# Kernel optimization log

Measured on AMD Instinct MI355X. Metric: run time of the kernel, lower is better.

## Reference

```python
import jax, jax.numpy as jnp
import numpy as np
from jax.ops import segment_sum

N = 100000      # nodes
E = 1600000     # edges
G = 128         # graphs in batch
D = 128         # input (embedding) dim
H = 128         # hidden dim
WALK = 16       # random-walk length
PED = 16        # PE embed dim
L = 5           # GNN layers
OUT = 10        # classes
EPS = 1e-5      # batchnorm eps


def setup_inputs() -> dict:
    key = jax.random.key(0)
    ks = jax.random.split(key, 32)
    f = lambda k, shp: (jax.random.normal(k, shp, dtype=jnp.float32) * 0.05)
    inp = {
        'x': jnp.zeros((N,), dtype=jnp.int64) if jax.config.jax_enable_x64 else jnp.zeros((N,), dtype=jnp.int32),
        'edge_index': jax.random.randint(ks[0], (2, E), 0, N),
        'batch': jnp.sort(jax.random.randint(ks[1], (N,), 0, G)),
        'emb_table': f(ks[2], (1, D)),
        'pe_w': f(ks[3], (WALK, PED)), 'pe_b': f(ks[4], (PED,)),
        'proj_w': f(ks[5], (D + PED, H)), 'proj_b': f(ks[6], (H,)),
        'gin_w1': f(ks[7], (L, H, H)), 'gin_b1': f(ks[8], (L, H)),
        'gin_w2': f(ks[9], (L, H, H)), 'gin_b2': f(ks[10], (L, H)),
        'bn_g': jnp.ones((L, H), jnp.float32), 'bn_b': jnp.zeros((L, H), jnp.float32),
        'ffn_w1': f(ks[11], (L, H, 2 * H)), 'ffn_b1': f(ks[12], (L, 2 * H)),
        'ffn_w2': f(ks[13], (L, 2 * H, H)), 'ffn_b2': f(ks[14], (L, H)),
        'ffn_bn_g': jnp.ones((L, H), jnp.float32), 'ffn_bn_b': jnp.zeros((L, H), jnp.float32),
        'out_w1': f(ks[15], (H, H)), 'out_b1': f(ks[16], (H,)),
        'out_w2': f(ks[17], (H, OUT)), 'out_b2': f(ks[18], (OUT,)),
    }
    return inp


def _batchnorm(h, g, b):
    # BatchNorm1d forward with batch statistics (training-mode math)
    mu = jnp.mean(h, axis=0)
    var = jnp.var(h, axis=0)
    return (h - mu) * jax.lax.rsqrt(var + EPS) * g + b


def _forward(emb_table, pe_w, pe_b, proj_w, proj_b, gin_w1, gin_b1, gin_w2, gin_b2,
             bn_g, bn_b, ffn_w1, ffn_b1, ffn_w2, ffn_b2, ffn_bn_g, ffn_bn_b,
             out_w1, out_b1, out_w2, out_b2, x, edge_index, batch):
    h0 = emb_table[x]                                # [N, D] (all indices are 0)

    # ---- RandomWalkPositionalEncoding (vectorized scatter-add per step) ----
    row0, col0 = edge_index[0], edge_index[1]
    loops = jnp.arange(N)
    row = jnp.concatenate([row0, loops])
    col = jnp.concatenate([col0, loops])             # self loops appended
    deg = segment_sum(jnp.ones(row.shape, jnp.float32), col, num_segments=N)
    dinv = jnp.where(deg > 0, jax.lax.rsqrt(jnp.maximum(deg, 1.0)), 0.0)
    norm_e = dinv[row] * dinv[col]                   # [E+N]

    cnt = segment_sum(jnp.ones((N,), jnp.float32), batch, num_segments=G)
    prob = 1.0 / jnp.maximum(cnt, 1.0)[batch]        # per-graph uniform init

    def rw_step(p, _):
        new_p = segment_sum(p[row] * norm_e, col, num_segments=N)
        return new_p * 0.9 + p * 0.1, p

    _, rw = jax.lax.scan(rw_step, prob, None, length=WALK)   # [WALK, N]
    pe = rw.T @ pe_w + pe_b                          # [N, PED]

    # ---- input projection ----
    h = jnp.concatenate([h0, pe], axis=-1) @ proj_w + proj_b # [N, H]

    # ---- stacked GIN layers with BN, residual and FFN (dropout = eval identity) ----
    for i in range(L):
        res = h
        agg = segment_sum(h[row0], col0, num_segments=N) + h  # GIN: (1+eps)x + sum_j x_j, eps=0
        z = jax.nn.relu(agg @ gin_w1[i] + gin_b1[i]) @ gin_w2[i] + gin_b2[i]
        z = jax.nn.relu(_batchnorm(z, bn_g[i], bn_b[i]))
        h = z + res
        res2 = h
        f = jax.nn.relu(h @ ffn_w1[i] + ffn_b1[i]) @ ffn_w2[i] + ffn_b2[i]
        h = _batchnorm(f + res2, ffn_bn_g[i], ffn_bn_b[i])

    # ---- global mean pooling + MLP head ----
    gsum = segment_sum(h, batch, num_segments=G)
    g = gsum / jnp.maximum(cnt, 1.0)[:, None]        # [G, H]
    out = jax.nn.relu(g @ out_w1 + out_b1) @ out_w2 + out_b2
    return out                                        # [G, OUT]


def reference(x, edge_index, batch, emb_table, pe_w, pe_b, proj_w, proj_b,
              gin_w1, gin_b1, gin_w2, gin_b2, bn_g, bn_b, ffn_w1, ffn_b1,
              ffn_w2, ffn_b2, ffn_bn_g, ffn_bn_b, out_w1, out_b1, out_w2, out_b2):
    return _forward(emb_table, pe_w, pe_b, proj_w, proj_b, gin_w1, gin_b1, gin_w2,
                    gin_b2, bn_g, bn_b, ffn_w1, ffn_b1, ffn_w2, ffn_b2,
                    ffn_bn_g, ffn_bn_b, out_w1, out_b1, out_w2, out_b2,
                    x, edge_index, batch)
```

## Files before the change

### kernel.cpp

```cpp
#include <hip/hip_runtime.h>
#include <math.h>

#define NN 100000
#define NE 1600000
#define NG 128
#define HD 128
#define WLK 16
#define NL 5
#define NOUT 10
#define BNEPS 1e-5f
#define CDIV(a,b) (((a)+(b)-1)/(b))

#define NBKT 782
#define NEB 400
#define EPB 4000
#define NSCAN (NBKT*NEB)
#define NSB CDIV(NSCAN,1024)
#define NBM 782

typedef float f32x4 __attribute__((ext_vector_type(4)));
typedef _Float16 f16x8 __attribute__((ext_vector_type(8)));
typedef unsigned short ushort_t;
typedef unsigned int uint_t;

__device__ __forceinline__ ushort_t f2h(float x) {
    union { _Float16 h; ushort_t u; } c;
    c.h = (_Float16)x;
    return c.u;
}
__device__ __forceinline__ float h2f(ushort_t u) {
    union { ushort_t u; _Float16 h; } c;
    c.u = u;
    return (float)c.h;
}

__global__ void k_cnt(const int* __restrict__ batch, int* __restrict__ cnt,
                      int* __restrict__ goff) {
    int g = threadIdx.x;
    if (g >= NG) return;
    int lo0 = 0, hi0 = NN;
    while (lo0 < hi0) { int m = (lo0 + hi0) >> 1; if (batch[m] < g) lo0 = m + 1; else hi0 = m; }
    int lo1 = lo0, hi1 = NN;
    while (lo1 < hi1) { int m = (lo1 + hi1) >> 1; if (batch[m] < g + 1) lo1 = m + 1; else hi1 = m; }
    cnt[g] = lo1 - lo0;
    goff[g] = lo0;
}

__global__ void k_bhist(const int* __restrict__ col0, int* __restrict__ bhist) {
    __shared__ int hist[NBKT];
    for (int i = threadIdx.x; i < NBKT; i += 256) hist[i] = 0;
    __syncthreads();
    int e0 = blockIdx.x * EPB;
    for (int e = e0 + threadIdx.x; e < e0 + EPB; e += 256) atomicAdd(&hist[col0[e] >> 7], 1);
    __syncthreads();
    for (int i = threadIdx.x; i < NBKT; i += 256) bhist[i * NEB + blockIdx.x] = hist[i];
}

__global__ void k_gscan1(const int* __restrict__ in, int* __restrict__ bsum) {
    __shared__ int sm[256];
    int base = blockIdx.x * 1024 + threadIdx.x * 4;
    int s = 0;
#pragma unroll
    for (int i = 0; i < 4; ++i) { int e = base + i; if (e < NSCAN) s += in[e]; }
    sm[threadIdx.x] = s; __syncthreads();
    for (int st = 128; st > 0; st >>= 1) {
        if (threadIdx.x < st) sm[threadIdx.x] += sm[threadIdx.x + st];
        __syncthreads();
    }
    if (threadIdx.x == 0) bsum[blockIdx.x] = sm[0];
}

__global__ void k_scan2(int* __restrict__ blksum, int nblk) {
    __shared__ int sm[512];
    int t = threadIdx.x;
    int x = (t < nblk) ? blksum[t] : 0;
    sm[t] = x; __syncthreads();
    for (int s = 1; s < 512; s <<= 1) {
        int v = (t >= s) ? sm[t - s] : 0;
        __syncthreads();
        sm[t] += v;
        __syncthreads();
    }
    if (t < nblk) blksum[t] = sm[t] - x;
}

__global__ void k_gscan3(const int* __restrict__ in, const int* __restrict__ bsum,
                         int* __restrict__ out) {
    __shared__ int sm[256];
    int t = threadIdx.x;
    int base = blockIdx.x * 1024 + t * 4;
    int v[4]; int s = 0;
#pragma unroll
    for (int i = 0; i < 4; ++i) { int e = base + i; v[i] = (e < NSCAN) ? in[e] : 0; s += v[i]; }
    sm[t] = s; __syncthreads();
    for (int st = 1; st < 256; st <<= 1) {
        int x = (t >= st) ? sm[t - st] : 0;
        __syncthreads();
        sm[t] += x;
        __syncthreads();
    }
    int excl = sm[t] - s + bsum[blockIdx.x];
#pragma unroll
    for (int i = 0; i < 4; ++i) { int e = base + i; if (e < NSCAN) { out[e] = excl; excl += v[i]; } }
}

__global__ void k_escatter(const int* __restrict__ row0, const int* __restrict__ col0,
                           const int* __restrict__ boffs, int2* __restrict__ epair) {
    __shared__ int cur[NBKT];
    for (int i = threadIdx.x; i < NBKT; i += 256) cur[i] = boffs[i * NEB + blockIdx.x];
    __syncthreads();
    int e0 = blockIdx.x * EPB;
    for (int e = e0 + threadIdx.x; e < e0 + EPB; e += 256) {
        int c = col0[e], r = row0[e];
        int pos = atomicAdd(&cur[c >> 7], 1);
        epair[pos] = make_int2(c, r);
    }
}

__global__ void k_bucket(const int2* __restrict__ epair, const int* __restrict__ boffs,
                         int* __restrict__ rowptr, int* __restrict__ deg,
                         int* __restrict__ esrc) {
    __shared__ int cnt_[128], scn[128], cur_[128];
    int bkt = blockIdx.x, t = threadIdx.x;
    int bs = boffs[bkt * NEB];
    int be = (bkt + 1 < NBKT) ? boffs[(bkt + 1) * NEB] : NE;
    if (t < 128) cnt_[t] = 0;
    __syncthreads();
    for (int e = bs + t; e < be; e += 256) atomicAdd(&cnt_[epair[e].x & 127], 1);
    __syncthreads();
    int c = (t < 128) ? cnt_[t] : 0;
    if (t < 128) scn[t] = c;
    __syncthreads();
    for (int st = 1; st < 128; st <<= 1) {
        int x = (t >= st && t < 128) ? scn[t - st] : 0;
        __syncthreads();
        if (t < 128) scn[t] += x;
        __syncthreads();
    }
    if (t < 128) {
        int excl = scn[t] - c;
        int node = bkt * 128 + t;
        if (node < NN) { rowptr[node] = bs + excl; deg[node] = c; }
        cur_[t] = bs + excl;
    }
    if (bkt == NBKT - 1 && t == 0) rowptr[NN] = NE;
    __syncthreads();
    for (int e = bs + t; e < be; e += 256) {
        int2 p = epair[e];
        int pos = atomicAdd(&cur_[p.x & 127], 1);
        esrc[pos] = p.y;
    }
}

__global__ void k_init_pe(const int* __restrict__ deg, const int* __restrict__ batch,
                          const int* __restrict__ cnt, float* __restrict__ dinv,
                          float* __restrict__ p, float* __restrict__ pd) {
    int v = blockIdx.x * 256 + threadIdx.x;
    if (v >= NN) return;
    float dv = rsqrtf((float)(deg[v] + 1));
    dinv[v] = dv;
    float pv = 1.0f / fmaxf((float)cnt[batch[v]], 1.0f);
    p[v] = pv; pd[v] = pv * dv;
}

__global__ void k_rw_step(const float* __restrict__ pin, const float* __restrict__ pdin,
                          const int* __restrict__ rowptr, const int* __restrict__ esrc,
                          const float* __restrict__ dinv, float* __restrict__ rwslice,
                          float* __restrict__ pout, float* __restrict__ pdout) {
    int v = blockIdx.x * 256 + threadIdx.x;
    if (v >= NN) return;
    int b = rowptr[v], e = rowptr[v + 1];
    float a[8];
#pragma unroll
    for (int k = 0; k < 8; ++k) a[k] = 0.f;
    int i = b;
    for (; i + 8 <= e; i += 8) {
        int s[8];
#pragma unroll
        for (int k = 0; k < 8; ++k) s[k] = esrc[i + k];
#pragma unroll
        for (int k = 0; k < 8; ++k) a[k] += pdin[s[k]];
    }
    for (; i < e; ++i) a[0] += pdin[esrc[i]];
    float s = ((a[0] + a[1]) + (a[2] + a[3])) + ((a[4] + a[5]) + (a[6] + a[7]));
    float dv = dinv[v];
    float pv = pin[v];
    float np = s * dv + pv * dv * dv;
    float nxt = 0.9f * np + 0.1f * pv;
    rwslice[v] = pv;
    pout[v] = nxt;
    pdout[v] = nxt * dv;
}

__global__ void k_mc1(const float* __restrict__ emb, const float* __restrict__ pe_w,
                      const float* __restrict__ pe_b, const float* __restrict__ proj_w,
                      const float* __restrict__ proj_b, float* __restrict__ M,
                      float* __restrict__ c1, float* __restrict__ bnA0,
                      float* __restrict__ bnB0) {
    int j = threadIdx.x;
    bnA0[j] = 1.f; bnB0[j] = 0.f;
    float c0 = proj_b[j];
    for (int d = 0; d < HD; ++d) c0 += emb[d] * proj_w[d * HD + j];
    for (int w = 0; w < WLK; ++w) c0 += pe_b[w] * proj_w[(HD + w) * HD + j];
    c1[j] = c0;
    for (int s = 0; s < WLK; ++s) {
        float m = 0.f;
        for (int w = 0; w < WLK; ++w) m += pe_w[s * WLK + w] * proj_w[(HD + w) * HD + j];
        M[s * HD + j] = m;
    }
}

__global__ void k_proj(const float* __restrict__ rw, const float* __restrict__ M,
                       const float* __restrict__ c1, uint2* __restrict__ th4) {
    int idx = blockIdx.x * 256 + threadIdx.x;
    if (idx >= NN * 32) return;
    int v = idx >> 5, cg = (idx & 31) * 4;
    float4 acc = *(const float4*)&c1[cg];
#pragma unroll
    for (int s = 0; s < WLK; ++s) {
        float r = rw[s * NN + v];
        float4 m = *(const float4*)&M[s * HD + cg];
        acc.x += r * m.x; acc.y += r * m.y; acc.z += r * m.z; acc.w += r * m.w;
    }
    th4[idx] = make_uint2((uint_t)f2h(acc.x) | ((uint_t)f2h(acc.y) << 16),
                          (uint_t)f2h(acc.z) | ((uint_t)f2h(acc.w) << 16));
}

__global__ void k_prepw(const float* __restrict__ g1, const float* __restrict__ g2,
                        const float* __restrict__ f1, const float* __restrict__ f2,
                        ushort_t* __restrict__ wt1, ushort_t* __restrict__ wt2,
                        ushort_t* __restrict__ wt3, ushort_t* __restrict__ wt4) {
    int i = blockIdx.x * 256 + threadIdx.x;
    if (i < 81920) {
        int l = i >> 14, rem = i & 16383, n = rem >> 7, k = rem & 127;
        wt1[i] = f2h(g1[l * 16384 + k * 128 + n]);
    } else if (i < 163840) {
        int j = i - 81920;
        int l = j >> 14, rem = j & 16383, n = rem >> 7, k = rem & 127;
        wt2[j] = f2h(g2[l * 16384 + k * 128 + n]);
    } else if (i < 327680) {
        int j = i - 163840;
        int l = j >> 15, rem = j & 32767, n = rem >> 7, k = rem & 127;
        wt3[j] = f2h(f1[l * 32768 + k * 256 + n]);
    } else {
        int j = i - 327680;
        int l = j >> 15, rem = j & 32767, n = rem >> 8, k = rem & 255;
        wt4[j] = f2h(f2[l * 32768 + k * 128 + n]);
    }
}

__global__ void k_aggb(const uint_t* __restrict__ th2, const int* __restrict__ rowptr,
                       const int* __restrict__ esrc, const float* __restrict__ bnA0,
                       const float* __restrict__ bnB0, uint_t* __restrict__ aggb2) {
    int wave = threadIdx.x >> 6, lane = threadIdx.x & 63;
    int v = blockIdx.x * 4 + wave;
    if (v >= NN) return;
    uint_t u = th2[(size_t)v * 64 + lane];
    float sx[8], sy[8];
#pragma unroll
    for (int k = 0; k < 8; ++k) { sx[k] = 0.f; sy[k] = 0.f; }
    sx[0] = h2f((ushort_t)(u & 0xFFFFu)); sy[0] = h2f((ushort_t)(u >> 16));
    int b = rowptr[v], e = rowptr[v + 1];
    int i = b;
    for (; i + 8 <= e; i += 8) {
        int idx[8]; uint_t x[8];
#pragma unroll
        for (int k = 0; k < 8; ++k) idx[k] = esrc[i + k];
#pragma unroll
        for (int k = 0; k < 8; ++k) x[k] = th2[(size_t)idx[k] * 64 + lane];
#pragma unroll
        for (int k = 0; k < 8; ++k) {
            sx[k] += h2f((ushort_t)(x[k] & 0xFFFFu));
            sy[k] += h2f((ushort_t)(x[k] >> 16));
        }
    }
    for (; i < e; ++i) {
        uint_t x = th2[(size_t)esrc[i] * 64 + lane];
        sx[0] += h2f((ushort_t)(x & 0xFFFFu)); sy[0] += h2f((ushort_t)(x >> 16));
    }
    float fx = ((sx[0] + sx[1]) + (sx[2] + sx[3])) + ((sx[4] + sx[5]) + (sx[6] + sx[7]));
    float fy = ((sy[0] + sy[1]) + (sy[2] + sy[3])) + ((sy[4] + sy[5]) + (sy[6] + sy[7]));
    float2 A = *(const float2*)&bnA0[lane * 2];
    float2 B = *(const float2*)&bnB0[lane * 2];
    float cf = (float)(e - b + 1);
    float ox = A.x * fx + cf * B.x;
    float oy = A.y * fy + cf * B.y;
    aggb2[(size_t)v * 64 + lane] = (uint_t)f2h(ox) | ((uint_t)f2h(oy) << 16);
}

#define GLDK 136
__global__ __launch_bounds__(256)
void k_gin(const ushort_t* __restrict__ A, const ushort_t* __restrict__ W1T,
           const ushort_t* __restrict__ W2T, const float* __restrict__ b1,
           const float* __restrict__ b2, ushort_t* __restrict__ z2h,
           float* __restrict__ partS, float* __restrict__ partQ) {
    __shared__ ushort_t As[128 * GLDK];
    __shared__ ushort_t Ws[64 * GLDK];
    __shared__ float sS[128], sQ[128];
    const int tid = threadIdx.x;
    const int w = tid >> 6, l = tid & 63;
    const int lm = l & 15, lq = l >> 4;
    const int rw0 = w * 32;
    const int vr0 = blockIdx.x * 128;
    if (tid < 128) { sS[tid] = 0.f; sQ[tid] = 0.f; }

#pragma unroll
    for (int it = 0; it < 8; ++it) {
        int f = it * 256 + tid;
        int row = f >> 4, sl = f & 15;
        uint4 a = make_uint4(0, 0, 0, 0);
        int vr = vr0 + row;
        if (vr < NN) a = *(const uint4*)&A[(size_t)vr * HD + sl * 8];
        *(uint4*)&As[row * GLDK + sl * 8] = a;
    }

    f32x4 z1a[2][2][4] = {};
    for (int c = 0; c < 2; ++c) {
        __syncthreads();
#pragma unroll
        for (int it = 0; it < 4; ++it) {
            int f = it * 256 + tid;
            int row = f >> 4, sl = f & 15;
            *(uint4*)&Ws[row * GLDK + sl * 8] =
                *(const uint4*)&W1T[(size_t)(c * 64 + row) * HD + sl * 8];
        }
        __syncthreads();
#pragma unroll
        for (int kk = 0; kk < 128; kk += 32) {
            f16x8 af[2], bf[4];
#pragma unroll
            for (int i = 0; i < 2; ++i)
                af[i] = *(const f16x8*)&As[(rw0 + i * 16 + lm) * GLDK + kk + lq * 8];
#pragma unroll
            for (int j = 0; j < 4; ++j)
                bf[j] = *(const f16x8*)&Ws[(j * 16 + lm) * GLDK + kk + lq * 8];
#pragma unroll
            for (int i = 0; i < 2; ++i)
#pragma unroll
                for (int j = 0; j < 4; ++j)
                    z1a[c][i][j] = __builtin_amdgcn_mfma_f32_16x16x32_f16(af[i], bf[j], z1a[c][i][j], 0, 0, 0);
        }
    }
    __syncthreads();

#pragma unroll
    for (int c = 0; c < 2; ++c)
#pragma unroll
        for (int j = 0; j < 4; ++j) {
            int col = c * 64 + j * 16 + lm;
            float bj = b1[col];
#pragma unroll
            for (int i = 0; i < 2; ++i)
#pragma unroll
                for (int r = 0; r < 4; ++r) {
                    int row = rw0 + i * 16 + lq * 4 + r;
                    As[row * GLDK + col] = f2h(fmaxf(z1a[c][i][j][r] + bj, 0.f));
                }
        }

    f32x4 z2a[2][2][4] = {};
    for (int c2 = 0; c2 < 2; ++c2) {
        __syncthreads();
#pragma unroll
        for (int it = 0; it < 4; ++it) {
            int f = it * 256 + tid;
            int row = f >> 4, sl = f & 15;
            *(uint4*)&Ws[row * GLDK + sl * 8] =
                *(const uint4*)&W2T[(size_t)(c2 * 64 + row) * HD + sl * 8];
        }
        __syncthreads();
#pragma unroll
        for (int kk = 0; kk < 128; kk += 32) {
            f16x8 af[2], bf[4];
#pragma unroll
            for (int i = 0; i < 2; ++i)
                af[i] = *(const f16x8*)&As[(rw0 + i * 16 + lm) * GLDK + kk + lq * 8];
#pragma unroll
            for (int j = 0; j < 4; ++j)
                bf[j] = *(const f16x8*)&Ws[(j * 16 + lm) * GLDK + kk + lq * 8];
#pragma unroll
            for (int i = 0; i < 2; ++i)
#pragma unroll
                for (int j = 0; j < 4; ++j)
                    z2a[c2][i][j] = __builtin_amdgcn_mfma_f32_16x16x32_f16(af[i], bf[j], z2a[c2][i][j], 0, 0, 0);
        }
    }

    float ls[2][4] = {}, lsq[2][4] = {};
#pragma unroll
    for (int c2 = 0; c2 < 2; ++c2)
#pragma unroll
        for (int j = 0; j < 4; ++j) {
            int col = c2 * 64 + j * 16 + lm;
            float bj = b2[col];
#pragma unroll
            for (int i = 0; i < 2; ++i)
#pragma unroll
                for (int r = 0; r < 4; ++r) {
                    int vr = vr0 + rw0 + i * 16 + lq * 4 + r;
                    if (vr < NN) {
                        float x = z2a[c2][i][j][r] + bj;
                        ls[c2][j] += x; lsq[c2][j] += x * x;
                        z2h[(size_t)vr * HD + col] = f2h(x);
                    }
                }
        }
#pragma unroll
    for (int c2 = 0; c2 < 2; ++c2)
#pragma unroll
        for (int j = 0; j < 4; ++j) {
            atomicAdd(&sS[c2 * 64 + j * 16 + lm], ls[c2][j]);
            atomicAdd(&sQ[c2 * 64 + j * 16 + lm], lsq[c2][j]);
        }
    __syncthreads();
    if (tid < 128) {
        partS[(size_t)tid * NBM + blockIdx.x] = sS[tid];
        partQ[(size_t)tid * NBM + blockIdx.x] = sQ[tid];
    }
}

#define FLDK 72
__global__ __launch_bounds__(256)
void k_ffn(ushort_t* __restrict__ th, const ushort_t* __restrict__ z2h,
           const ushort_t* __restrict__ W3T, const float* __restrict__ b3,
           const ushort_t* __restrict__ W4T, const float* __restrict__ b4,
           const float* __restrict__ bnA0, const float* __restrict__ bnB0,
           const float* __restrict__ bnA1, const float* __restrict__ bnB1,
           float* __restrict__ partS, float* __restrict__ partQ) {
    __shared__ ushort_t As[128 * GLDK];
    __shared__ ushort_t Fs[128 * FLDK];
    __shared__ ushort_t Ws[128 * FLDK];
    __shared__ float sS[128], sQ[128];
    __shared__ float sA0[128], sB0[128], sA1[128], sB1[128];
    const int tid = threadIdx.x;
    const int w = tid >> 6, l = tid & 63;
    const int lm = l & 15, lq = l >> 4;
    const int rw0 = w * 32;
    const int vr0 = blockIdx.x * 128;

    if (tid < 128) {
        sS[tid] = 0.f; sQ[tid] = 0.f;
        sA0[tid] = bnA0[tid]; sB0[tid] = bnB0[tid];
        sA1[tid] = bnA1[tid]; sB1[tid] = bnB1[tid];
    }
    __syncthreads();

#pragma unroll
    for (int it = 0; it < 8; ++it) {
        int f = it * 256 + tid;
        int row = f >> 4, sl = f & 15;
        int vr = vr0 + row;
        uint4 o = make_uint4(0, 0, 0, 0);
        if (vr < NN) {
            uint4 tv = *(const uint4*)&th[(size_t)vr * HD + sl * 8];
            uint4 zv = *(const uint4*)&z2h[(size_t)vr * HD + sl * 8];
            uint_t tu[4] = {tv.x, tv.y, tv.z, tv.w};
            uint_t zu[4] = {zv.x, zv.y, zv.z, zv.w};
            uint_t ou[4];
#pragma unroll
            for (int m = 0; m < 4; ++m) {
                int ch0 = sl * 8 + m * 2;
                float t0 = h2f((ushort_t)(tu[m] & 0xFFFFu));
                float t1 = h2f((ushort_t)(tu[m] >> 16));
                float z0 = h2f((ushort_t)(zu[m] & 0xFFFFu));
                float z1 = h2f((ushort_t)(zu[m] >> 16));
                float h0 = sA0[ch0] * t0 + sB0[ch0] + fmaxf(sA1[ch0] * z0 + sB1[ch0], 0.f);
                float h1 = sA0[ch0 + 1] * t1 + sB0[ch0 + 1] + fmaxf(sA1[ch0 + 1] * z1 + sB1[ch0 + 1], 0.f);
                ou[m] = (uint_t)f2h(h0) | ((uint_t)f2h(h1) << 16);
            }
            o = make_uint4(ou[0], ou[1], ou[2], ou[3]);
        }
        *(uint4*)&As[row * GLDK + sl * 8] = o;
    }

    f32x4 acc2[2][2][4] = {};
    for (int kc = 0; kc < 4; ++kc) {
        __syncthreads();
#pragma unroll
        for (int it = 0; it < 4; ++it) {
            int f = it * 256 + tid;
            int row = f >> 4, sl = f & 15;
            *(uint4*)&Ws[row * GLDK + sl * 8] =
                *(const uint4*)&W3T[(size_t)(kc * 64 + row) * HD + sl * 8];
        }
        __syncthreads();
        f32x4 f1a[2][4] = {};
#pragma unroll
        for (int kk = 0; kk < 128; kk += 32) {
            f16x8 af[2], bf[4];
#pragma unroll
            for (int i = 0; i < 2; ++i)
                af[i] = *(const f16x8*)&As[(rw0 + i * 16 + lm) * GLDK + kk + lq * 8];
#pragma unroll
            for (int j = 0; j < 4; ++j)
                bf[j] = *(const f16x8*)&Ws[(j * 16 + lm) * GLDK + kk + lq * 8];
#pragma unroll
            for (int i = 0; i < 2; ++i)
#pragma unroll
                for (int j = 0; j < 4; ++j)
                    f1a[i][j] = __builtin_amdgcn_mfma_f32_16x16x32_f16(af[i], bf[j], f1a[i][j], 0, 0, 0);
        }
#pragma unroll
        for (int j = 0; j < 4; ++j) {
            int fcol = j * 16 + lm;
            float bj = b3[kc * 64 + fcol];
#pragma unroll
            for (int i = 0; i < 2; ++i)
#pragma unroll
                for (int r = 0; r < 4; ++r) {
                    int row = rw0 + i * 16 + lq * 4 + r;
                    Fs[row * FLDK + fcol] = f2h(fmaxf(f1a[i][j][r] + bj, 0.f));
                }
        }
        __syncthreads();
#pragma unroll
        for (int it = 0; it < 4; ++it) {
            int f = it * 256 + tid;
            int row = f >> 3, sl = f & 7;
            *(uint4*)&Ws[row * FLDK + sl * 8] =
                *(const uint4*)&W4T[(size_t)row * 256 + kc * 64 + sl * 8];
        }
        __syncthreads();
#pragma unroll
        for (int kk = 0; kk < 64; kk += 32) {
            f16x8 af[2];
#pragma unroll
            for (int i = 0; i < 2; ++i)
                af[i] = *(const f16x8*)&Fs[(rw0 + i * 16 + lm) * FLDK + kk + lq * 8];
#pragma unroll
            for (int c2 = 0; c2 < 2; ++c2)
#pragma unroll
                for (int j = 0; j < 4; ++j) {
                    f16x8 bf = *(const f16x8*)&Ws[(c2 * 64 + j * 16 + lm) * FLDK + kk + lq * 8];
#pragma unroll
                    for (int i = 0; i < 2; ++i)
                        acc2[c2][i][j] = __builtin_amdgcn_mfma_f32_16x16x32_f16(af[i], bf, acc2[c2][i][j], 0, 0, 0);
                }
        }
    }

    float ls[2][4] = {}, lsq[2][4] = {};
#pragma unroll
    for (int c2 = 0; c2 < 2; ++c2)
#pragma unroll
        for (int j = 0; j < 4; ++j) {
            int col = c2 * 64 + j * 16 + lm;
            float bj = b4[col];
#pragma unroll
            for (int i = 0; i < 2; ++i)
#pragma unroll
                for (int r = 0; r < 4; ++r) {
                    int lrow = rw0 + i * 16 + lq * 4 + r;
                    int vr = vr0 + lrow;
                    if (vr < NN) {
                        float resv = h2f(As[lrow * GLDK + col]);
                        float x = acc2[c2][i][j][r] + bj + resv;
                        ls[c2][j] += x; lsq[c2][j] += x * x;
                        th[(size_t)vr * HD + col] = f2h(x);
                    }
                }
        }
#pragma unroll
    for (int c2 = 0; c2 < 2; ++c2)
#pragma unroll
        for (int j = 0; j < 4; ++j) {
            atomicAdd(&sS[c2 * 64 + j * 16 + lm], ls[c2][j]);
            atomicAdd(&sQ[c2 * 64 + j * 16 + lm], lsq[c2][j]);
        }
    __syncthreads();
    if (tid < 128) {
        partS[(size_t)tid * NBM + blockIdx.x] = sS[tid];
        partQ[(size_t)tid * NBM + blockIdx.x] = sQ[tid];
    }
}

__global__ void k_bnparm(const float* __restrict__ partS, const float* __restrict__ partQ,
                         const float* __restrict__ g, const float* __restrict__ b,
                         float* __restrict__ bnA, float* __restrict__ bnB) {
    __shared__ float smS[256], smQ[256];
    int c = blockIdx.x, t = threadIdx.x;
    float s = 0.f, q = 0.f;
    for (int i = t; i < NBM; i += 256) {
        s += partS[(size_t)c * NBM + i];
        q += partQ[(size_t)c * NBM + i];
    }
    smS[t] = s; smQ[t] = q; __syncthreads();
    for (int st = 128; st > 0; st >>= 1) {
        if (t < st) { smS[t] += smS[t + st]; smQ[t] += smQ[t + st]; }
        __syncthreads();
    }
    if (t == 0) {
        float mu = smS[0] * (1.0f / NN);
        float var = smQ[0] * (1.0f / NN) - mu * mu;
        float inv = rsqrtf(var + BNEPS);
        float a = g[c] * inv;
        bnA[c] = a;
        bnB[c] = b[c] - mu * a;
    }
}

__global__ void k_pool(const uint2* __restrict__ th4, const int* __restrict__ goff,
                       const int* __restrict__ cnt, float* __restrict__ gsum) {
    __shared__ float4 sm[256];
    int g = blockIdx.x >> 2, sub = blockIdx.x & 3;
    int n0 = goff[g], n = cnt[g];
    int cg = threadIdx.x & 31, rl = threadIdx.x >> 5;
    float4 acc = make_float4(0.f, 0.f, 0.f, 0.f);
    for (int r = sub * 8 + rl; r < n; r += 32) {
        uint2 v = th4[(size_t)(n0 + r) * 32 + cg];
        acc.x += h2f((ushort_t)(v.x & 0xFFFFu));
        acc.y += h2f((ushort_t)(v.x >> 16));
        acc.z += h2f((ushort_t)(v.y & 0xFFFFu));
        acc.w += h2f((ushort_t)(v.y >> 16));
    }
    sm[threadIdx.x] = acc; __syncthreads();
    for (int st = 128; st >= 32; st >>= 1) {
        if (threadIdx.x < st) {
            float4 o = sm[threadIdx.x + st];
            sm[threadIdx.x].x += o.x; sm[threadIdx.x].y += o.y;
            sm[threadIdx.x].z += o.z; sm[threadIdx.x].w += o.w;
        }
        __syncthreads();
    }
    if (threadIdx.x < 32) {
        float4 v = sm[threadIdx.x];
        atomicAdd(&gsum[g * HD + cg * 4 + 0], v.x);
        atomicAdd(&gsum[g * HD + cg * 4 + 1], v.y);
        atomicAdd(&gsum[g * HD + cg * 4 + 2], v.z);
        atomicAdd(&gsum[g * HD + cg * 4 + 3], v.w);
    }
}

__global__ void k_head(const float* __restrict__ gsum, const int* __restrict__ cnt,
                       const float* __restrict__ bnA0, const float* __restrict__ bnB0,
                       const float* __restrict__ w1, const float* __restrict__ b1,
                       const float* __restrict__ w2, const float* __restrict__ b2,
                       float* __restrict__ out) {
    __shared__ float gv[HD], av[HD];
    int gid = blockIdx.x, t = threadIdx.x;
    float c = fmaxf((float)cnt[gid], 1.0f);
    gv[t] = bnA0[t] * (gsum[gid * HD + t] / c) + bnB0[t];
    __syncthreads();
    float a = b1[t];
    for (int k = 0; k < HD; ++k) a += gv[k] * w1[k * HD + t];
    av[t] = fmaxf(a, 0.f);
    __syncthreads();
    if (t < NOUT) {
        float o = b2[t];
        for (int k = 0; k < HD; ++k) o += av[k] * w2[k * NOUT + t];
        out[gid * NOUT + t] = o;
    }
}

static constexpr size_t AL(size_t x) { return (x + 511) & ~(size_t)511; }
static constexpr size_t OFF_TH     = 0;
static constexpr size_t OFF_SHARE  = OFF_TH     + AL((size_t)NN * HD * 2);
static constexpr size_t SZ_SHARE   = AL((size_t)NN * HD * 2);
static constexpr size_t OFF_Z2     = OFF_SHARE  + SZ_SHARE;
static constexpr size_t OFF_RW     = OFF_Z2     + AL((size_t)NN * HD * 2);
static constexpr size_t OFF_P0     = OFF_RW     + AL((size_t)WLK * NN * 4);
static constexpr size_t OFF_P1     = OFF_P0     + AL((size_t)NN * 4);
static constexpr size_t OFF_PD0    = OFF_P1     + AL((size_t)NN * 4);
static constexpr size_t OFF_PD1    = OFF_PD0    + AL((size_t)NN * 4);
static constexpr size_t OFF_DINV   = OFF_PD1    + AL((size_t)NN * 4);
static constexpr size_t OFF_ESRC   = OFF_DINV   + AL((size_t)NN * 4);
static constexpr size_t OFF_ROWPTR = OFF_ESRC   + AL((size_t)NE * 4);
static constexpr size_t OFF_DEG    = OFF_ROWPTR + AL((size_t)(NN + 1) * 4);
static constexpr size_t OFF_BHIST  = OFF_DEG    + AL((size_t)NN * 4);
static constexpr size_t OFF_BOFFS  = OFF_BHIST  + AL((size_t)NSCAN * 4);
static constexpr size_t OFF_BSUM   = OFF_BOFFS  + AL((size_t)NSCAN * 4);
static constexpr size_t OFF_WT1    = OFF_BSUM   + AL(512 * 4);
static constexpr size_t OFF_WT2    = OFF_WT1    + AL((size_t)5 * 16384 * 2);
static constexpr size_t OFF_WT3    = OFF_WT2    + AL((size_t)5 * 16384 * 2);
static constexpr size_t OFF_WT4    = OFF_WT3    + AL((size_t)5 * 32768 * 2);
static constexpr size_t OFF_PARTS  = OFF_WT4    + AL((size_t)5 * 32768 * 2);
static constexpr size_t OFF_PARTQ  = OFF_PARTS  + AL((size_t)128 * NBM * 4);
static constexpr size_t OFF_BNA0   = OFF_PARTQ  + AL((size_t)128 * NBM * 4);
static constexpr size_t OFF_BNB0   = OFF_BNA0   + AL(128 * 4);
static constexpr size_t OFF_BNA1   = OFF_BNB0   + AL(128 * 4);
static constexpr size_t OFF_BNB1   = OFF_BNA1   + AL(128 * 4);
static constexpr size_t OFF_M      = OFF_BNB1   + AL(128 * 4);
static constexpr size_t OFF_C1     = OFF_M      + AL((size_t)WLK * HD * 4);
static constexpr size_t OFF_CNT    = OFF_C1     + AL(HD * 4);
static constexpr size_t OFF_GOFF   = OFF_CNT    + AL(NG * 4);
static constexpr size_t OFF_GSUM   = OFF_GOFF   + AL(NG * 4);
static constexpr size_t ZERO_BYTES = (size_t)NG * HD * 4;

extern "C" void kernel_launch(void* const* d_in, const int* in_sizes, int n_in,
                              void* d_out, int out_size, void* d_ws, size_t ws_size,
                              hipStream_t stream) {
    const int* eidx = (const int*)d_in[1];
    const int* row0 = eidx;
    const int* col0 = eidx + NE;
    const int* batch = (const int*)d_in[2];
    const float* emb = (const float*)d_in[3];
    const float* pe_w = (const float*)d_in[4];
    const float* pe_b = (const float*)d_in[5];
    const float* proj_w = (const float*)d_in[6];
    const float* proj_b = (const float*)d_in[7];
    const float* gin_w1 = (const float*)d_in[8];
    const float* gin_b1 = (const float*)d_in[9];
    const float* gin_w2 = (const float*)d_in[10];
    const float* gin_b2 = (const float*)d_in[11];
    const float* bn_g = (const float*)d_in[12];
    const float* bn_b = (const float*)d_in[13];
    const float* ffn_w1 = (const float*)d_in[14];
    const float* ffn_b1 = (const float*)d_in[15];
    const float* ffn_w2 = (const float*)d_in[16];
    const float* ffn_b2 = (const float*)d_in[17];
    const float* ffn_bn_g = (const float*)d_in[18];
    const float* ffn_bn_b = (const float*)d_in[19];
    const float* out_w1 = (const float*)d_in[20];
    const float* out_b1 = (const float*)d_in[21];
    const float* out_w2 = (const float*)d_in[22];
    const float* out_b2 = (const float*)d_in[23];
    float* out = (float*)d_out;

    char* ws = (char*)d_ws;
    ushort_t* th    = (ushort_t*)(ws + OFF_TH);
    ushort_t* aggh  = (ushort_t*)(ws + OFF_SHARE);
    int2*     epair = (int2*)(ws + OFF_SHARE);
    ushort_t* z2h   = (ushort_t*)(ws + OFF_Z2);
    float*    rw    = (float*)(ws + OFF_RW);
    float*    p0    = (float*)(ws + OFF_P0);
    float*    p1    = (float*)(ws + OFF_P1);
    float*    pd0   = (float*)(ws + OFF_PD0);
    float*    pd1   = (float*)(ws + OFF_PD1);
    float*    dinv  = (float*)(ws + OFF_DINV);
    int*      esrc  = (int*)(ws + OFF_ESRC);
    int*      rowptr= (int*)(ws + OFF_ROWPTR);
    int*      deg   = (int*)(ws + OFF_DEG);
    int*      bhist = (int*)(ws + OFF_BHIST);
    int*      boffs = (int*)(ws + OFF_BOFFS);
    int*      bsum  = (int*)(ws + OFF_BSUM);
    ushort_t* wt1   = (ushort_t*)(ws + OFF_WT1);
    ushort_t* wt2   = (ushort_t*)(ws + OFF_WT2);
    ushort_t* wt3   = (ushort_t*)(ws + OFF_WT3);
    ushort_t* wt4   = (ushort_t*)(ws + OFF_WT4);
    float*    partS = (float*)(ws + OFF_PARTS);
    float*    partQ = (float*)(ws + OFF_PARTQ);
    float*    bnA0  = (float*)(ws + OFF_BNA0);
    float*    bnB0  = (float*)(ws + OFF_BNB0);
    float*    bnA1  = (float*)(ws + OFF_BNA1);
    float*    bnB1  = (float*)(ws + OFF_BNB1);
    float*    M     = (float*)(ws + OFF_M);
    float*    c1    = (float*)(ws + OFF_C1);
    int*      cnt   = (int*)(ws + OFF_CNT);
    int*      goff  = (int*)(ws + OFF_GOFF);
    float*    gsum  = (float*)(ws + OFF_GSUM);

    const int NB = CDIV(NN, 256);
    const int NBV = CDIV(NN * 32, 256);

    hipMemsetAsync(ws + OFF_GSUM, 0, ZERO_BYTES, stream);

    k_cnt<<<1, 128, 0, stream>>>(batch, cnt, goff);
    k_bhist<<<NEB, 256, 0, stream>>>(col0, bhist);
    k_gscan1<<<NSB, 256, 0, stream>>>(bhist, bsum);
    k_scan2<<<1, 512, 0, stream>>>(bsum, NSB);
    k_gscan3<<<NSB, 256, 0, stream>>>(bhist, bsum, boffs);
    k_escatter<<<NEB, 256, 0, stream>>>(row0, col0, boffs, epair);
    k_bucket<<<NBKT, 256, 0, stream>>>(epair, boffs, rowptr, deg, esrc);

    k_init_pe<<<NB, 256, 0, stream>>>(deg, batch, cnt, dinv, p0, pd0);
    k_mc1<<<1, 128, 0, stream>>>(emb, pe_w, pe_b, proj_w, proj_b, M, c1, bnA0, bnB0);
    k_prepw<<<1920, 256, 0, stream>>>(gin_w1, gin_w2, ffn_w1, ffn_w2, wt1, wt2, wt3, wt4);
    for (int s = 0; s < WLK; ++s) {
        const float* pin = (s & 1) ? p1 : p0;
        const float* pdin = (s & 1) ? pd1 : pd0;
        float* pout = (s & 1) ? p0 : p1;
        float* pdout = (s & 1) ? pd0 : pd1;
        k_rw_step<<<NB, 256, 0, stream>>>(pin, pdin, rowptr, esrc, dinv,
                                          rw + (size_t)s * NN, pout, pdout);
    }
    k_proj<<<NBV, 256, 0, stream>>>(rw, M, c1, (uint2*)th);

    for (int i = 0; i < NL; ++i) {
        k_aggb<<<CDIV(NN, 4), 256, 0, stream>>>((const uint_t*)th, rowptr, esrc,
                                                bnA0, bnB0, (uint_t*)aggh);
        k_gin<<<NBM, 256, 0, stream>>>(aggh, wt1 + (size_t)i * 16384, wt2 + (size_t)i * 16384,
                                       gin_b1 + i * HD, gin_b2 + i * HD, z2h, partS, partQ);
        k_bnparm<<<128, 256, 0, stream>>>(partS, partQ, bn_g + i * HD, bn_b + i * HD, bnA1, bnB1);
        k_ffn<<<NBM, 256, 0, stream>>>(th, z2h, wt3 + (size_t)i * 32768, ffn_b1 + i * 256,
                                       wt4 + (size_t)i * 32768, ffn_b2 + i * HD,
                                       bnA0, bnB0, bnA1, bnB1, partS, partQ);
        k_bnparm<<<128, 256, 0, stream>>>(partS, partQ, ffn_bn_g + i * HD, ffn_bn_b + i * HD,
                                          bnA0, bnB0);
    }

    k_pool<<<NG * 4, 256, 0, stream>>>((const uint2*)th, goff, cnt, gsum);
    k_head<<<NG, 128, 0, stream>>>(gsum, cnt, bnA0, bnB0, out_w1, out_b1, out_w2, out_b2, out);
}
```

Before: 1.440 ms.

## Fuse random-walk steps into persistent kernel and fold BN stats into last block

Replaces the 16 per-step random-walk launches with a single persistent kernel of 391 blocks that uses a grid-wide atomic counter barrier between steps. It also removes the separate k_bnparm launches by having the last-finishing block of k_gin and k_ffn reduce the partial sums and compute the BN scale and shift. The goal is to cut kernel launch and tail overhead, but the spin barrier assumes all 391 blocks are co-resident, and the last-block reduction runs serially over 782 partials per channel. It also slightly restructures the fp16 stores into shared memory.

```diff
diff --git a/kernel.cpp b/kernel.cpp
--- a/kernel.cpp
+++ b/kernel.cpp
@@ -17,6 +17,7 @@
 #define NSCAN (NBKT*NEB)
 #define NSB CDIV(NSCAN,1024)
 #define NBM 782
+#define NBRW 391
 
 typedef float f32x4 __attribute__((ext_vector_type(4)));
 typedef _Float16 f16x8 __attribute__((ext_vector_type(8)));
@@ -163,33 +164,52 @@
     p[v] = pv; pd[v] = pv * dv;
 }
 
-__global__ void k_rw_step(const float* __restrict__ pin, const float* __restrict__ pdin,
-                          const int* __restrict__ rowptr, const int* __restrict__ esrc,
-                          const float* __restrict__ dinv, float* __restrict__ rwslice,
-                          float* __restrict__ pout, float* __restrict__ pdout) {
+__global__ void k_rw_all(float* __restrict__ p0, float* __restrict__ p1,
+                         float* __restrict__ pd0, float* __restrict__ pd1,
+                         const int* __restrict__ rowptr, const int* __restrict__ esrc,
+                         const float* __restrict__ dinv, float* __restrict__ rw,
+                         int* __restrict__ ctr) {
     int v = blockIdx.x * 256 + threadIdx.x;
-    if (v >= NN) return;
-    int b = rowptr[v], e = rowptr[v + 1];
-    float a[8];
-#pragma unroll
-    for (int k = 0; k < 8; ++k) a[k] = 0.f;
-    int i = b;
-    for (; i + 8 <= e; i += 8) {
-        int s[8];
-#pragma unroll
-        for (int k = 0; k < 8; ++k) s[k] = esrc[i + k];
-#pragma unroll
-        for (int k = 0; k < 8; ++k) a[k] += pdin[s[k]];
-    }
-    for (; i < e; ++i) a[0] += pdin[esrc[i]];
-    float s = ((a[0] + a[1]) + (a[2] + a[3])) + ((a[4] + a[5]) + (a[6] + a[7]));
-    float dv = dinv[v];
-    float pv = pin[v];
-    float np = s * dv + pv * dv * dv;
-    float nxt = 0.9f * np + 0.1f * pv;
-    rwslice[v] = pv;
-    pout[v] = nxt;
-    pdout[v] = nxt * dv;
+    bool act = (v < NN);
+    int b = 0, e = 0;
+    float dv = 0.f;
+    if (act) { b = rowptr[v]; e = rowptr[v + 1]; dv = dinv[v]; }
+    for (int s = 0; s < WLK; ++s) {
+        const float* pin  = (s & 1) ? p1 : p0;
+        const float* pdin = (s & 1) ? pd1 : pd0;
+        float* pout  = (s & 1) ? p0 : p1;
+        float* pdout = (s & 1) ? pd0 : pd1;
+        if (act) {
+            float a[8];
+#pragma unroll
+            for (int k = 0; k < 8; ++k) a[k] = 0.f;
+            int i = b;
+            for (; i + 8 <= e; i += 8) {
+                int sv[8];
+#pragma unroll
+                for (int k = 0; k < 8; ++k) sv[k] = esrc[i + k];
+#pragma unroll
+                for (int k = 0; k < 8; ++k) a[k] += pdin[sv[k]];
+            }
+            for (; i < e; ++i) a[0] += pdin[esrc[i]];
+            float sum = ((a[0] + a[1]) + (a[2] + a[3])) + ((a[4] + a[5]) + (a[6] + a[7]));
+            float pv = pin[v];
+            float np = sum * dv + pv * dv * dv;
+            float nxt = 0.9f * np + 0.1f * pv;
+            rw[(size_t)s * NN + v] = pv;
+            pout[v] = nxt;
+            pdout[v] = nxt * dv;
+        }
+        if (s == WLK - 1) break;
+        __threadfence();
+        __syncthreads();
+        if (threadIdx.x == 0) {
+            __hip_atomic_fetch_add(&ctr[s], 1, __ATOMIC_ACQ_REL, __HIP_MEMORY_SCOPE_AGENT);
+            while (__hip_atomic_load(&ctr[s], __ATOMIC_ACQUIRE, __HIP_MEMORY_SCOPE_AGENT) < NBRW)
+                __builtin_amdgcn_s_sleep(2);
+        }
+        __syncthreads();
+    }
 }
 
 __global__ void k_mc1(const float* __restrict__ emb, const float* __restrict__ pe_w,
@@ -288,12 +308,47 @@
     aggb2[(size_t)v * 64 + lane] = (uint_t)f2h(ox) | ((uint_t)f2h(oy) << 16);
 }
 
+__device__ __forceinline__ void bn_lastblock(int tid, float* sS, float* sQ,
+                                             const float* __restrict__ partS,
+                                             const float* __restrict__ partQ,
+                                             const float* __restrict__ g,
+                                             const float* __restrict__ b,
+                                             float* __restrict__ bnA,
+                                             float* __restrict__ bnB,
+                                             int* __restrict__ ctr) {
+    __threadfence();
+    __shared__ int isLast;
+    if (tid == 0) {
+        int old = __hip_atomic_fetch_add(ctr, 1, __ATOMIC_ACQ_REL, __HIP_MEMORY_SCOPE_AGENT);
+        isLast = (old == NBM - 1);
+    }
+    __syncthreads();
+    if (!isLast) return;
+    float s = 0.f;
+    const float* src = (tid < 128) ? (partS + (size_t)tid * NBM)
+                                   : (partQ + (size_t)(tid - 128) * NBM);
+    for (int i = 0; i < NBM; ++i) s += src[i];
+    if (tid < 128) sS[tid] = s; else sQ[tid - 128] = s;
+    __syncthreads();
+    if (tid < 128) {
+        float mu = sS[tid] * (1.0f / NN);
+        float var = sQ[tid] * (1.0f / NN) - mu * mu;
+        float inv = rsqrtf(var + BNEPS);
+        float a = g[tid] * inv;
+        bnA[tid] = a;
+        bnB[tid] = b[tid] - mu * a;
+    }
+}
+
 #define GLDK 136
 __global__ __launch_bounds__(256)
 void k_gin(const ushort_t* __restrict__ A, const ushort_t* __restrict__ W1T,
            const ushort_t* __restrict__ W2T, const float* __restrict__ b1,
            const float* __restrict__ b2, ushort_t* __restrict__ z2h,
-           float* __restrict__ partS, float* __restrict__ partQ) {
+           float* __restrict__ partS, float* __restrict__ partQ,
+           const float* __restrict__ gBN, const float* __restrict__ bBN,
+           float* __restrict__ bnA1, float* __restrict__ bnB1,
+           int* __restrict__ ctr) {
     __shared__ ushort_t As[128 * GLDK];
     __shared__ ushort_t Ws[64 * GLDK];
     __shared__ float sS[128], sQ[128];
@@ -350,12 +405,11 @@
             int col = c * 64 + j * 16 + lm;
             float bj = b1[col];
 #pragma unroll
-            for (int i = 0; i < 2; ++i)
-#pragma unroll
-                for (int r = 0; r < 4; ++r) {
-                    int row = rw0 + i * 16 + lq * 4 + r;
-                    As[row * GLDK + col] = f2h(fmaxf(z1a[c][i][j][r] + bj, 0.f));
-                }
+            for (int r = 0; r < 4; ++r) {
+                int row0_ = rw0 + lq * 4 + r;
+                As[row0_ * GLDK + col] = f2h(fmaxf(z1a[c][0][j][r] + bj, 0.f));
+                As[(row0_ + 16) * GLDK + col] = f2h(fmaxf(z1a[c][1][j][r] + bj, 0.f));
+            }
         }
 
     f32x4 z2a[2][2][4] = {};
@@ -417,6 +471,8 @@
         partS[(size_t)tid * NBM + blockIdx.x] = sS[tid];
         partQ[(size_t)tid * NBM + blockIdx.x] = sQ[tid];
     }
+    __syncthreads();
+    bn_lastblock(tid, sS, sQ, partS, partQ, gBN, bBN, bnA1, bnB1, ctr);
 }
 
 #define FLDK 72
@@ -426,7 +482,10 @@
            const ushort_t* __restrict__ W4T, const float* __restrict__ b4,
            const float* __restrict__ bnA0, const float* __restrict__ bnB0,
            const float* __restrict__ bnA1, const float* __restrict__ bnB1,
-           float* __restrict__ partS, float* __restrict__ partQ) {
+           float* __restrict__ partS, float* __restrict__ partQ,
+           const float* __restrict__ gBN, const float* __restrict__ bBN,
+           float* __restrict__ obnA, float* __restrict__ obnB,
+           int* __restrict__ ctr) {
     __shared__ ushort_t As[128 * GLDK];
     __shared__ ushort_t Fs[128 * FLDK];
     __shared__ ushort_t Ws[128 * FLDK];
@@ -505,12 +564,11 @@
             int fcol = j * 16 + lm;
             float bj = b3[kc * 64 + fcol];
 #pragma unroll
-            for (int i = 0; i < 2; ++i)
-#pragma unroll
-                for (int r = 0; r < 4; ++r) {
-                    int row = rw0 + i * 16 + lq * 4 + r;
-                    Fs[row * FLDK + fcol] = f2h(fmaxf(f1a[i][j][r] + bj, 0.f));
-                }
+            for (int r = 0; r < 4; ++r) {
+                int row0_ = rw0 + lq * 4 + r;
+                Fs[row0_ * FLDK + fcol] = f2h(fmaxf(f1a[0][j][r] + bj, 0.f));
+                Fs[(row0_ + 16) * FLDK + fcol] = f2h(fmaxf(f1a[1][j][r] + bj, 0.f));
+            }
         }
         __syncthreads();
 #pragma unroll
@@ -572,31 +630,8 @@
         partS[(size_t)tid * NBM + blockIdx.x] = sS[tid];
         partQ[(size_t)tid * NBM + blockIdx.x] = sQ[tid];
     }
-}
-
-__global__ void k_bnparm(const float* __restrict__ partS, const float* __restrict__ partQ,
-                         const float* __restrict__ g, const float* __restrict__ b,
-                         float* __restrict__ bnA, float* __restrict__ bnB) {
-    __shared__ float smS[256], smQ[256];
-    int c = blockIdx.x, t = threadIdx.x;
-    float s = 0.f, q = 0.f;
-    for (int i = t; i < NBM; i += 256) {
-        s += partS[(size_t)c * NBM + i];
-        q += partQ[(size_t)c * NBM + i];
-    }
-    smS[t] = s; smQ[t] = q; __syncthreads();
-    for (int st = 128; st > 0; st >>= 1) {
-        if (t < st) { smS[t] += smS[t + st]; smQ[t] += smQ[t + st]; }
-        __syncthreads();
-    }
-    if (t == 0) {
-        float mu = smS[0] * (1.0f / NN);
-        float var = smQ[0] * (1.0f / NN) - mu * mu;
-        float inv = rsqrtf(var + BNEPS);
-        float a = g[c] * inv;
-        bnA[c] = a;
-        bnB[c] = b[c] - mu * a;
-    }
+    __syncthreads();
+    bn_lastblock(tid, sS, sQ, partS, partQ, gBN, bBN, obnA, obnB, ctr);
 }
 
 __global__ void k_pool(const uint2* __restrict__ th4, const int* __restrict__ goff,
@@ -684,7 +719,8 @@
 static constexpr size_t OFF_CNT    = OFF_C1     + AL(HD * 4);
 static constexpr size_t OFF_GOFF   = OFF_CNT    + AL(NG * 4);
 static constexpr size_t OFF_GSUM   = OFF_GOFF   + AL(NG * 4);
-static constexpr size_t ZERO_BYTES = (size_t)NG * HD * 4;
+static constexpr size_t OFF_CTR    = OFF_GSUM   + AL((size_t)NG * HD * 4);
+static constexpr size_t ZERO_BYTES = (OFF_CTR - OFF_GSUM) + 26 * 4;
 
 extern "C" void kernel_launch(void* const* d_in, const int* in_sizes, int n_in,
                               void* d_out, int out_size, void* d_ws, size_t ws_size,
@@ -748,6 +784,7 @@
     int*      cnt   = (int*)(ws + OFF_CNT);
     int*      goff  = (int*)(ws + OFF_GOFF);
     float*    gsum  = (float*)(ws + OFF_GSUM);
+    int*      sctr  = (int*)(ws + OFF_CTR);
 
     const int NB = CDIV(NN, 256);
     const int NBV = CDIV(NN * 32, 256);
@@ -765,27 +802,20 @@
     k_init_pe<<<NB, 256, 0, stream>>>(deg, batch, cnt, dinv, p0, pd0);
     k_mc1<<<1, 128, 0, stream>>>(emb, pe_w, pe_b, proj_w, proj_b, M, c1, bnA0, bnB0);
     k_prepw<<<1920, 256, 0, stream>>>(gin_w1, gin_w2, ffn_w1, ffn_w2, wt1, wt2, wt3, wt4);
-    for (int s = 0; s < WLK; ++s) {
-        const float* pin = (s & 1) ? p1 : p0;
-        const float* pdin = (s & 1) ? pd1 : pd0;
-        float* pout = (s & 1) ? p0 : p1;
-        float* pdout = (s & 1) ? pd0 : pd1;
-        k_rw_step<<<NB, 256, 0, stream>>>(pin, pdin, rowptr, esrc, dinv,
-                                          rw + (size_t)s * NN, pout, pdout);
-    }
+    k_rw_all<<<NBRW, 256, 0, stream>>>(p0, p1, pd0, pd1, rowptr, esrc, dinv, rw, sctr + 10);
     k_proj<<<NBV, 256, 0, stream>>>(rw, M, c1, (uint2*)th);
 
     for (int i = 0; i < NL; ++i) {
         k_aggb<<<CDIV(NN, 4), 256, 0, stream>>>((const uint_t*)th, rowptr, esrc,
                                                 bnA0, bnB0, (uint_t*)aggh);
         k_gin<<<NBM, 256, 0, stream>>>(aggh, wt1 + (size_t)i * 16384, wt2 + (size_t)i * 16384,
-                                       gin_b1 + i * HD, gin_b2 + i * HD, z2h, partS, partQ);
-        k_bnparm<<<128, 256, 0, stream>>>(partS, partQ, bn_g + i * HD, bn_b + i * HD, bnA1, bnB1);
+                                       gin_b1 + i * HD, gin_b2 + i * HD, z2h, partS, partQ,
+                                       bn_g + i * HD, bn_b + i * HD, bnA1, bnB1, sctr + i);
         k_ffn<<<NBM, 256, 0, stream>>>(th, z2h, wt3 + (size_t)i * 32768, ffn_b1 + i * 256,
                                        wt4 + (size_t)i * 32768, ffn_b2 + i * HD,
-                                       bnA0, bnB0, bnA1, bnB1, partS, partQ);
-        k_bnparm<<<128, 256, 0, stream>>>(partS, partQ, ffn_bn_g + i * HD, ffn_bn_b + i * HD,
-                                          bnA0, bnB0);
+                                       bnA0, bnB0, bnA1, bnB1, partS, partQ,
+                                       ffn_bn_g + i * HD, ffn_bn_b + i * HD, bnA0, bnB0,
+                                       sctr + 5 + i);
     }
 
     k_pool<<<NG * 4, 256, 0, stream>>>((const uint2*)th, goff, cnt, gsum);
```

After: 4.150 ms. +188.2%, slower.
